# Optimization experiments

Measured on AMD Instinct MI355X. Metric: run time of the kernel, lower is better.

Reference implementation:

```python
import jax, jax.numpy as jnp
import numpy as np

N_NODES = 250_000
N_EDGES = 1_250_000
N_CRY = 50_000
EMB = 200
FEA = 64
HID = 256
N_GRAPH = 3
ELEM_HEADS = 3
CRY_HEADS = 3


def _simple_net(x, w1, b1, w2, b2):
    # SimpleNetwork([d_in, 256, d_out]): Linear -> LeakyReLU -> Linear
    h = jax.nn.leaky_relu(x @ w1 + b1, negative_slope=0.01)
    return h @ w2 + b2


def setup_inputs() -> dict:
    key = jax.random.key(0)
    ks = jax.random.split(key, 32)
    s = 0.05
    inp = {
        # weights strictly positive (fractional stoichiometry weights)
        "elem_weights": jax.random.uniform(ks[0], (N_NODES, 1), jnp.float32) * 0.9 + 0.05,
        "elem_fea": jax.random.normal(ks[1], (N_NODES, EMB), jnp.float32),
        "self_fea_idx": jax.random.randint(ks[2], (N_EDGES,), 0, N_NODES),
        "nbr_fea_idx": jax.random.randint(ks[3], (N_EDGES,), 0, N_NODES),
        "cry_elem_idx": jnp.sort(jax.random.randint(ks[4], (N_NODES,), 0, N_CRY)),
        # embedding: Linear(EMB, FEA-1)
        "emb_w": jax.random.normal(ks[5], (EMB, FEA - 1), jnp.float32) * s,
        "emb_b": jnp.zeros((FEA - 1,), jnp.float32),
        # graph-layer attention heads (n_graph, elem_heads, ...)
        "g_gate_w1": jax.random.normal(ks[6], (N_GRAPH, ELEM_HEADS, 2 * FEA, HID), jnp.float32) * s,
        "g_gate_b1": jnp.zeros((N_GRAPH, ELEM_HEADS, HID), jnp.float32),
        "g_gate_w2": jax.random.normal(ks[7], (N_GRAPH, ELEM_HEADS, HID, 1), jnp.float32) * s,
        "g_gate_b2": jnp.zeros((N_GRAPH, ELEM_HEADS, 1), jnp.float32),
        "g_msg_w1": jax.random.normal(ks[8], (N_GRAPH, ELEM_HEADS, 2 * FEA, HID), jnp.float32) * s,
        "g_msg_b1": jnp.zeros((N_GRAPH, ELEM_HEADS, HID), jnp.float32),
        "g_msg_w2": jax.random.normal(ks[9], (N_GRAPH, ELEM_HEADS, HID, FEA), jnp.float32) * s,
        "g_msg_b2": jnp.zeros((N_GRAPH, ELEM_HEADS, FEA), jnp.float32),
        "g_pow": jax.random.normal(ks[10], (N_GRAPH, ELEM_HEADS), jnp.float32),
        # crystal pooling heads
        "c_gate_w1": jax.random.normal(ks[11], (CRY_HEADS, FEA, HID), jnp.float32) * s,
        "c_gate_b1": jnp.zeros((CRY_HEADS, HID), jnp.float32),
        "c_gate_w2": jax.random.normal(ks[12], (CRY_HEADS, HID, 1), jnp.float32) * s,
        "c_gate_b2": jnp.zeros((CRY_HEADS, 1), jnp.float32),
        "c_msg_w1": jax.random.normal(ks[13], (CRY_HEADS, FEA, HID), jnp.float32) * s,
        "c_msg_b1": jnp.zeros((CRY_HEADS, HID), jnp.float32),
        "c_msg_w2": jax.random.normal(ks[14], (CRY_HEADS, HID, FEA), jnp.float32) * s,
        "c_msg_b2": jnp.zeros((CRY_HEADS, FEA), jnp.float32),
        "c_pow": jax.random.normal(ks[15], (CRY_HEADS,), jnp.float32),
    }
    return inp


def _attn_pool(fea, weights, index, num_segments, gw1, gb1, gw2, gb2, mw1, mb1, mw2, mb2, p):
    # WeightedAttentionPooling: scatter-softmax with (weights ** pow) factor
    gate = _simple_net(fea, gw1, gb1, gw2, gb2)                       # (E, 1)
    gmax = jax.ops.segment_max(gate, index, num_segments=num_segments)
    gate = (weights ** p) * jnp.exp(gate - gmax[index])
    den = jax.ops.segment_sum(gate, index, num_segments=num_segments)
    gate = gate / (den[index] + 1e-10)
    msg = _simple_net(fea, mw1, mb1, mw2, mb2)                        # (E, FEA)
    return jax.ops.segment_sum(gate * msg, index, num_segments=num_segments)


def reference(elem_weights, elem_fea, self_fea_idx, nbr_fea_idx, cry_elem_idx,
              emb_w, emb_b,
              g_gate_w1, g_gate_b1, g_gate_w2, g_gate_b2,
              g_msg_w1, g_msg_b1, g_msg_w2, g_msg_b2, g_pow,
              c_gate_w1, c_gate_b1, c_gate_w2, c_gate_b2,
              c_msg_w1, c_msg_b1, c_msg_w2, c_msg_b2, c_pow):
    n = elem_fea.shape[0]
    x = elem_fea @ emb_w + emb_b                                      # (N, FEA-1)
    x = jnp.concatenate([x, elem_weights], axis=1)                    # (N, FEA)
    w_nbr = elem_weights[nbr_fea_idx]                                 # (M, 1)
    for l in range(g_pow.shape[0]):
        fea = jnp.concatenate([x[self_fea_idx], x[nbr_fea_idx]], axis=1)  # (M, 2*FEA)
        heads = []
        for h in range(g_pow.shape[1]):
            heads.append(_attn_pool(
                fea, w_nbr, self_fea_idx, n,
                g_gate_w1[l, h], g_gate_b1[l, h], g_gate_w2[l, h], g_gate_b2[l, h],
                g_msg_w1[l, h], g_msg_b1[l, h], g_msg_w2[l, h], g_msg_b2[l, h],
                g_pow[l, h]))
        x = jnp.mean(jnp.stack(heads), axis=0) + x                    # residual
    heads = []
    for h in range(c_pow.shape[0]):
        heads.append(_attn_pool(
            x, elem_weights, cry_elem_idx, N_CRY,
            c_gate_w1[h], c_gate_b1[h], c_gate_w2[h], c_gate_b2[h],
            c_msg_w1[h], c_msg_b1[h], c_msg_w2[h], c_msg_b2[h],
            c_pow[h]))
    return jnp.mean(jnp.stack(heads), axis=0)                         # (C, FEA)
```

## Files before the change

kernel.cpp:

```cpp
#include <hip/hip_runtime.h>
#include <math.h>

#define NN 250000
#define NE 1250000
#define NC 50000
#define EMBD 200
#define NCH 245
#define NBLK 22000
#define SSTR ((size_t)NBLK * 64)

typedef unsigned int u32;
typedef unsigned short u16;
typedef short s16x8 __attribute__((ext_vector_type(8)));
typedef float f32x4 __attribute__((ext_vector_type(4)));

__device__ __forceinline__ u16 f2bf(float f) {
    u32 u = __float_as_uint(f);
    return (u16)((u + 0x7FFFu + ((u >> 16) & 1u)) >> 16);
}
__device__ __forceinline__ float bf2f(u16 u) { return __uint_as_float(((u32)u) << 16); }
__device__ __forceinline__ u32 cvtpk(float lo, float hi) {
    u32 r;
    asm("v_cvt_pk_bf16_f32 %0, %1, %2" : "=v"(r) : "v"(lo), "v"(hi));
    return r;
}
__device__ __forceinline__ float lrelu(float v) { return v > 0.f ? v : 0.01f * v; }
__device__ __forceinline__ u32 encf(float f) {
    u32 u = __float_as_uint(f);
    return (u & 0x80000000u) ? ~u : (u | 0x80000000u);
}
__device__ __forceinline__ float decf(u32 k) {
    return __uint_as_float((k & 0x80000000u) ? (k ^ 0x80000000u) : ~k);
}

__global__ void k_pack(const float* __restrict__ src, u16* __restrict__ dst,
                       int K, int N, int nheads)
{
    const int t = blockIdx.x * 256 + threadIdx.x;
    const int F = (K / 32) * (N / 16);
    if (t >= nheads * F * 64) return;
    const int lane = t & 63;
    const int fh = t >> 6;
    const int f = fh % F, head = fh / F;
    const int ng = f % (N / 16), ks = f / (N / 16);
    const int q = lane >> 4, c = lane & 15;
    const float* s = src + (size_t)head * K * N;
    u16 o[8];
    #pragma unroll
    for (int i = 0; i < 8; ++i)
        o[i] = f2bf(s[(size_t)(32 * ks + 8 * q + i) * N + 16 * ng + c]);
    uint4 v;
    v.x = (u32)o[0] | ((u32)o[1] << 16);
    v.y = (u32)o[2] | ((u32)o[3] << 16);
    v.z = (u32)o[4] | ((u32)o[5] << 16);
    v.w = (u32)o[6] | ((u32)o[7] << 16);
    *(uint4*)(dst + (size_t)head * K * N + ((size_t)f * 64 + lane) * 8) = v;
}

__global__ void k_packe(const float* __restrict__ src, u16* __restrict__ dst)
{
    const int t = blockIdx.x * 256 + threadIdx.x;
    if (t >= 28 * 64) return;
    const int lane = t & 63, f = t >> 6;
    const int ng = f & 3, ks = f >> 2;
    const int q = lane >> 4, c = lane & 15;
    u16 o[8];
    #pragma unroll
    for (int i = 0; i < 8; ++i) {
        const int kr = 32 * ks + 8 * q + i;
        const int col = 16 * ng + c;
        o[i] = (kr < EMBD && col < 63) ? f2bf(src[kr * 63 + col]) : (u16)0;
    }
    uint4 v;
    v.x = (u32)o[0] | ((u32)o[1] << 16);
    v.y = (u32)o[2] | ((u32)o[3] << 16);
    v.z = (u32)o[4] | ((u32)o[5] << 16);
    v.w = (u32)o[6] | ((u32)o[7] << 16);
    *(uint4*)(dst + ((size_t)f * 64 + lane) * 8) = v;
}

__global__ void k_pack2(const float* __restrict__ src, u16* __restrict__ dst, int nheads)
{
    const int t = blockIdx.x * 256 + threadIdx.x;
    const int F = 32;
    if (t >= nheads * F * 64) return;
    const int lane = t & 63;
    const int fh = t >> 6;
    const int f = fh % F, head = fh / F;
    const int ks2 = f >> 2, ng = f & 3;
    const int q = lane >> 4, c = lane & 15;
    const int half = ks2 >> 2, k2l = ks2 & 3;
    const float* s = src + (size_t)head * 256 * 64;
    u16 o[8];
    #pragma unroll
    for (int i = 0; i < 8; ++i) {
        const int pl = 32 * k2l + 8 * q + i;
        const int krow = (pl >> 5) * 64 + (2 * half + (pl & 1)) * 16 + ((pl >> 1) & 15);
        o[i] = f2bf(s[(size_t)krow * 64 + 16 * ng + c]);
    }
    uint4 v;
    v.x = (u32)o[0] | ((u32)o[1] << 16);
    v.y = (u32)o[2] | ((u32)o[3] << 16);
    v.z = (u32)o[4] | ((u32)o[5] << 16);
    v.w = (u32)o[6] | ((u32)o[7] << 16);
    *(uint4*)(dst + (size_t)head * 256 * 64 + ((size_t)f * 64 + lane) * 8) = v;
}

__global__ __launch_bounds__(256) void k_embed_mm(
    const float* __restrict__ elem_fea, const float* __restrict__ elem_w,
    const u16* __restrict__ webp, const float* __restrict__ emb_b,
    float* __restrict__ x, u16* __restrict__ xbf)
{
    __shared__ __align__(16) u16 Ahi[64 * 256];
    __shared__ __align__(16) u16 Alo[64 * 256];
    const int tid = threadIdx.x;
    const int n0 = blockIdx.x * 64;

    for (int i = tid; i < 64 * 3; i += 256) {
        const int row = i / 3, j = 25 + i % 3;
        uint4 z; z.x = 0; z.y = 0; z.z = 0; z.w = 0;
        *(uint4*)((char*)Ahi + row * 512 + ((j ^ (row & 7)) * 16)) = z;
        *(uint4*)((char*)Alo + row * 512 + ((j ^ (row & 7)) * 16)) = z;
    }
    for (int i = tid; i < 64 * 50; i += 256) {
        const int row = i / 50, f4 = i % 50;
        const int node = min(n0 + row, NN - 1);
        float4 v = *(const float4*)(elem_fea + (size_t)node * EMBD + f4 * 4);
        const u16 h0 = f2bf(v.x), h1 = f2bf(v.y), h2 = f2bf(v.z), h3 = f2bf(v.w);
        uint2 hi, lo;
        hi.x = (u32)h0 | ((u32)h1 << 16);
        hi.y = (u32)h2 | ((u32)h3 << 16);
        lo.x = (u32)f2bf(v.x - bf2f(h0)) | ((u32)f2bf(v.y - bf2f(h1)) << 16);
        lo.y = (u32)f2bf(v.z - bf2f(h2)) | ((u32)f2bf(v.w - bf2f(h3)) << 16);
        const int off = row * 512 + (((f4 >> 1) ^ (row & 7)) * 16) + (f4 & 1) * 8;
        *(uint2*)((char*)Ahi + off) = hi;
        *(uint2*)((char*)Alo + off) = lo;
    }
    __syncthreads();

    const int w = tid >> 6, lane = tid & 63, q = lane >> 4, c = lane & 15;
    s16x8 B[7];
    #pragma unroll
    for (int ks = 0; ks < 7; ++ks)
        B[ks] = *(const s16x8*)(webp + ((size_t)(ks * 4 + w) * 64 + lane) * 8);
    f32x4 acc[4];
    #pragma unroll
    for (int m = 0; m < 4; ++m) acc[m] = 0.f;
    #pragma unroll
    for (int ks = 0; ks < 7; ++ks) {
        #pragma unroll
        for (int m = 0; m < 4; ++m) {
            const int row = m * 16 + c;
            const int g = (ks * 4 + q) ^ (row & 7);
            s16x8 ah = *(const s16x8*)((const char*)Ahi + row * 512 + g * 16);
            s16x8 al = *(const s16x8*)((const char*)Alo + row * 512 + g * 16);
            acc[m] = __builtin_amdgcn_mfma_f32_16x16x32_bf16(ah, B[ks], acc[m], 0, 0, 0);
            acc[m] = __builtin_amdgcn_mfma_f32_16x16x32_bf16(al, B[ks], acc[m], 0, 0, 0);
        }
    }
    const int col = w * 16 + c;
    const float bv = (col < 63) ? emb_b[col] : 0.f;
    #pragma unroll
    for (int m = 0; m < 4; ++m)
        #pragma unroll
        for (int r = 0; r < 4; ++r) {
            const int node = n0 + m * 16 + q * 4 + r;
            if (node < NN) {
                const float val = (col < 63) ? acc[m][r] + bv : elem_w[node];
                x[(size_t)node * 64 + col] = val;
                xbf[(size_t)node * 64 + col] = f2bf(val);
            }
        }
}

__global__ void k_deg(const int* __restrict__ self_idx, int* __restrict__ deg) {
    int e = blockIdx.x * 256 + threadIdx.x;
    if (e < NE) atomicAdd(&deg[self_idx[e]], 1);
}

__global__ void k_nodepack(const int* __restrict__ deg, int* __restrict__ nstart,
                           int* __restrict__ ctotal)
{
    __shared__ int sdeg[1024];
    __shared__ int sst[1024];
    const int c0 = blockIdx.x << 10;
    const int cnt = min(1024, NN - c0);
    for (int i = threadIdx.x; i < cnt; i += 64) sdeg[i] = deg[c0 + i];
    __syncthreads();
    if (threadIdx.x == 0) {
        int cur = 0;
        for (int i = 0; i < cnt; ++i) {
            int d = sdeg[i];
            if (d > 0 && ((cur & 63) + d > 64)) cur = (cur + 63) & ~63;
            sst[i] = cur;
            cur += d;
        }
        ctotal[blockIdx.x] = (cur + 63) & ~63;
    }
    __syncthreads();
    for (int i = threadIdx.x; i < cnt; i += 64) nstart[c0 + i] = sst[i];
}

__global__ void k_chunkscan(const int* __restrict__ ctotal, int* __restrict__ cbase) {
    __shared__ int s[256];
    int t = threadIdx.x;
    int v = (t < NCH) ? ctotal[t] : 0;
    s[t] = v;
    __syncthreads();
    for (int off = 1; off < 256; off <<= 1) {
        int add = (t >= off) ? s[t - off] : 0;
        __syncthreads();
        s[t] += add;
        __syncthreads();
    }
    if (t < NCH) cbase[t] = s[t] - v;
}

__global__ void k_fill(const int* __restrict__ self_idx, const int* __restrict__ nstart,
                       const int* __restrict__ cbase, int* __restrict__ cursor,
                       int* __restrict__ eslot)
{
    int e = blockIdx.x * 256 + threadIdx.x;
    if (e >= NE) return;
    int n = self_idx[e];
    int r = atomicAdd(&cursor[n], 1);
    eslot[cbase[n >> 10] + nstart[n] + r] = e;
}

__global__ __launch_bounds__(256, 4) void k_lgate(
    const u16* __restrict__ xbf, const int* __restrict__ eslot,
    const int* __restrict__ sidx, const int* __restrict__ nidx,
    const float* __restrict__ elem_w,
    const u16* __restrict__ gw1p, const float* __restrict__ gb1,
    const float* __restrict__ gw2, const float* __restrict__ gpw,
    float* __restrict__ sgf_out)
{
    __shared__ __align__(16) u16 sA[64 * 128];
    __shared__ float sg[4][64];
    __shared__ float gfin[64], tval[64];
    __shared__ float swn[64];
    __shared__ int   snid[64];
    __shared__ short srs[64], sre[64];
    const int tid = threadIdx.x;
    const int base = blockIdx.x * 64;
    if (eslot[base] < 0) return;

    if (tid < 64) {
        int e = eslot[base + tid];
        snid[tid] = (e >= 0) ? sidx[e] : -1;
        swn[tid] = (e >= 0) ? elem_w[nidx[e]] : 1.f;
    }
    for (int i = tid; i < 64 * 16; i += 256) {
        const int row = i >> 4, g = i & 15;
        const int e = eslot[base + row];
        uint4 v; v.x = 0; v.y = 0; v.z = 0; v.w = 0;
        if (e >= 0) {
            const int node = (g < 8) ? sidx[e] : nidx[e];
            v = *(const uint4*)(xbf + (size_t)node * 64 + (g & 7) * 8);
        }
        *(uint4*)((char*)sA + row * 256 + ((g ^ (row & 7)) * 16)) = v;
    }
    __syncthreads();
    if (tid < 64) {
        int n = snid[tid];
        int rs = tid, re = tid + 1;
        if (n >= 0) {
            while (rs > 0 && snid[rs - 1] == n) --rs;
            while (re < 64 && snid[re] == n) ++re;
        }
        srs[tid] = (short)rs; sre[tid] = (short)re;
    }

    const int w = tid >> 6, lane = tid & 63, q = lane >> 4, c = lane & 15;

    #pragma unroll 1
    for (int h = 0; h < 3; ++h) {
        float part[4][4];
        #pragma unroll
        for (int m = 0; m < 4; ++m)
            #pragma unroll
            for (int r = 0; r < 4; ++r) part[m][r] = 0.f;
        const u16* wp = gw1p + (size_t)h * 128 * 256;
        #pragma unroll 1
        for (int half = 0; half < 2; ++half) {
            f32x4 acc[4][2];
            #pragma unroll
            for (int m = 0; m < 4; ++m) { acc[m][0] = 0.f; acc[m][1] = 0.f; }
            __builtin_amdgcn_s_setprio(1);
            #pragma unroll 2
            for (int ks = 0; ks < 4; ++ks) {
                s16x8 B1[2];
                #pragma unroll
                for (int n2 = 0; n2 < 2; ++n2)
                    B1[n2] = *(const s16x8*)(wp + ((size_t)(ks * 16 + w * 4 + half * 2 + n2) * 64 + lane) * 8);
                s16x8 a[4];
                #pragma unroll
                for (int m = 0; m < 4; ++m) {
                    const int row = m * 16 + c;
                    a[m] = *(const s16x8*)((const char*)sA + row * 256 + (((ks * 4 + q) ^ (row & 7)) * 16));
                }
                #pragma unroll
                for (int n2 = 0; n2 < 2; ++n2)
                    #pragma unroll
                    for (int m = 0; m < 4; ++m)
                        acc[m][n2] = __builtin_amdgcn_mfma_f32_16x16x32_bf16(a[m], B1[n2], acc[m][n2], 0, 0, 0);
            }
            __builtin_amdgcn_s_setprio(0);
            #pragma unroll
            for (int n2 = 0; n2 < 2; ++n2) {
                const int col = w * 64 + (half * 2 + n2) * 16 + c;
                const float b1v = gb1[h * 256 + col];
                const float w2v = gw2[h * 256 + col];
                #pragma unroll
                for (int m = 0; m < 4; ++m)
                    #pragma unroll
                    for (int r = 0; r < 4; ++r)
                        part[m][r] += lrelu(acc[m][n2][r] + b1v) * w2v;
            }
        }
        #pragma unroll
        for (int off = 1; off < 16; off <<= 1)
            #pragma unroll
            for (int m = 0; m < 4; ++m)
                #pragma unroll
                for (int r = 0; r < 4; ++r)
                    part[m][r] += __shfl_xor(part[m][r], off, 64);
        if (c == 0) {
            #pragma unroll
            for (int m = 0; m < 4; ++m)
                #pragma unroll
                for (int r = 0; r < 4; ++r)
                    sg[w][m * 16 + q * 4 + r] = part[m][r];
        }
        __syncthreads();
        if (tid < 64)
            gfin[tid] = (snid[tid] >= 0) ? sg[0][tid] + sg[1][tid] + sg[2][tid] + sg[3][tid] : -1e30f;
        __syncthreads();
        if (tid < 64) {
            const int rs = srs[tid], re = sre[tid];
            float m = -1e30f;
            for (int j = rs; j < re; ++j) m = fmaxf(m, gfin[j]);
            tval[tid] = (snid[tid] >= 0) ? powf(swn[tid], gpw[h]) * expf(gfin[tid] - m) : 0.f;
        }
        __syncthreads();
        if (tid < 64) {
            const int rs = srs[tid], re = sre[tid];
            float d = 1e-10f;
            for (int j = rs; j < re; ++j) d += tval[j];
            sgf_out[SSTR * h + base + tid] = tval[tid] / d;
        }
        __syncthreads();
    }
}

__global__ __launch_bounds__(256, 4) void k_lmsg(
    const u16* __restrict__ xbf, const int* __restrict__ eslot,
    const int* __restrict__ sidx, const int* __restrict__ nidx,
    const u16* __restrict__ mw1p, const float* __restrict__ mb1,
    const u16* __restrict__ mw2p, const float* __restrict__ mb2,
    const float* __restrict__ sgf_in, float* __restrict__ pooled)
{
    __shared__ __align__(16) u16 sA[64 * 128];
    __shared__ __align__(16) u16 sH[64 * 128];
    __shared__ float sgfl[64][3];
    __shared__ int   snid[64];
    __shared__ short srs[64], sre[64];
    const int tid = threadIdx.x;
    const int base = blockIdx.x * 64;
    if (eslot[base] < 0) return;

    if (tid < 64) {
        int e = eslot[base + tid];
        snid[tid] = (e >= 0) ? sidx[e] : -1;
    }
    if (tid < 192) {
        const int row = tid / 3, h = tid % 3;
        sgfl[row][h] = sgf_in[SSTR * h + base + row];
    }
    for (int i = tid; i < 64 * 16; i += 256) {
        const int row = i >> 4, g = i & 15;
        const int e = eslot[base + row];
        uint4 v; v.x = 0; v.y = 0; v.z = 0; v.w = 0;
        if (e >= 0) {
            const int node = (g < 8) ? sidx[e] : nidx[e];
            v = *(const uint4*)(xbf + (size_t)node * 64 + (g & 7) * 8);
        }
        *(uint4*)((char*)sA + row * 256 + ((g ^ (row & 7)) * 16)) = v;
    }
    __syncthreads();
    if (tid < 64) {
        int n = snid[tid];
        int rs = tid, re = tid + 1;
        if (n >= 0) {
            while (rs > 0 && snid[rs - 1] == n) --rs;
            while (re < 64 && snid[re] == n) ++re;
        }
        srs[tid] = (short)rs; sre[tid] = (short)re;
    }

    const int w = tid >> 6, lane = tid & 63, q = lane >> 4, c = lane & 15;
    float wacc[4][4];
    #pragma unroll
    for (int m = 0; m < 4; ++m)
        #pragma unroll
        for (int r = 0; r < 4; ++r) wacc[m][r] = 0.f;

    #pragma unroll 1
    for (int h = 0; h < 3; ++h) {
        const u16* wp = mw1p + (size_t)h * 128 * 256;
        #pragma unroll 1
        for (int half = 0; half < 2; ++half) {
            f32x4 acc[4][2];
            #pragma unroll
            for (int m = 0; m < 4; ++m) { acc[m][0] = 0.f; acc[m][1] = 0.f; }
            __builtin_amdgcn_s_setprio(1);
            #pragma unroll 2
            for (int ks = 0; ks < 4; ++ks) {
                s16x8 B1[2];
                #pragma unroll
                for (int n2 = 0; n2 < 2; ++n2)
                    B1[n2] = *(const s16x8*)(wp + ((size_t)(ks * 16 + w * 4 + half * 2 + n2) * 64 + lane) * 8);
                s16x8 a[4];
                #pragma unroll
                for (int m = 0; m < 4; ++m) {
                    const int row = m * 16 + c;
                    a[m] = *(const s16x8*)((const char*)sA + row * 256 + (((ks * 4 + q) ^ (row & 7)) * 16));
                }
                #pragma unroll
                for (int n2 = 0; n2 < 2; ++n2)
                    #pragma unroll
                    for (int m = 0; m < 4; ++m)
                        acc[m][n2] = __builtin_amdgcn_mfma_f32_16x16x32_bf16(a[m], B1[n2], acc[m][n2], 0, 0, 0);
            }
            __builtin_amdgcn_s_setprio(0);

            __syncthreads();
            const float b1a = mb1[h * 256 + w * 64 + (half * 2 + 0) * 16 + c];
            const float b1b = mb1[h * 256 + w * 64 + (half * 2 + 1) * 16 + c];
            #pragma unroll
            for (int m = 0; m < 4; ++m)
                #pragma unroll
                for (int r = 0; r < 4; ++r) {
                    const int row = m * 16 + q * 4 + r;
                    const u32 pk = cvtpk(lrelu(acc[m][0][r] + b1a), lrelu(acc[m][1][r] + b1b));
                    *(u32*)((char*)sH + row * 256 + (((w * 4 + (c >> 2)) ^ (row & 7)) * 16) + (c & 3) * 4) = pk;
                }
            s16x8 B2[4];
            #pragma unroll
            for (int k2 = 0; k2 < 4; ++k2)
                B2[k2] = *(const s16x8*)(mw2p + (size_t)h * 256 * 64 + ((size_t)((half * 4 + k2) * 4 + w) * 64 + lane) * 8);
            __syncthreads();

            f32x4 acc2[4];
            #pragma unroll
            for (int m = 0; m < 4; ++m) acc2[m] = 0.f;
            __builtin_amdgcn_s_setprio(1);
            #pragma unroll
            for (int k2 = 0; k2 < 4; ++k2) {
                #pragma unroll
                for (int m2 = 0; m2 < 4; ++m2) {
                    const int row = m2 * 16 + c;
                    s16x8 a2 = *(const s16x8*)((const char*)sH + row * 256 + (((k2 * 4 + q) ^ (row & 7)) * 16));
                    acc2[m2] = __builtin_amdgcn_mfma_f32_16x16x32_bf16(a2, B2[k2], acc2[m2], 0, 0, 0);
                }
            }
            __builtin_amdgcn_s_setprio(0);
            const float b2v = half ? mb2[h * 64 + w * 16 + c] : 0.f;
            #pragma unroll
            for (int m2 = 0; m2 < 4; ++m2)
                #pragma unroll
                for (int r = 0; r < 4; ++r) {
                    const int row = m2 * 16 + q * 4 + r;
                    wacc[m2][r] += (acc2[m2][r] + b2v) * sgfl[row][h];
                }
        }
        __syncthreads();
    }

    float* waccL = (float*)sH;
    #pragma unroll
    for (int m = 0; m < 4; ++m)
        #pragma unroll
        for (int r = 0; r < 4; ++r)
            waccL[(m * 16 + q * 4 + r) * 64 + w * 16 + c] = wacc[m][r];
    __syncthreads();
    {
        const int col = tid & 63, grp = tid >> 6;
        for (int i = grp; i < 64; i += 4) {
            const int n = snid[i];
            if (n >= 0 && srs[i] == (short)i) {
                float s = 0.f;
                const int re = sre[i];
                for (int j = i; j < re; ++j) s += waccL[j * 64 + col];
                pooled[(size_t)n * 64 + col] = s * (1.f / 3.f);
            }
        }
    }
}

__global__ void k_mirror2(float* __restrict__ x, const float* __restrict__ pooled,
                          u16* __restrict__ xbf, int n4)
{
    int i = blockIdx.x * 256 + threadIdx.x;
    if (i >= n4) return;
    float4 xv = *(const float4*)(x + (size_t)i * 4);
    float4 pv = *(const float4*)(pooled + (size_t)i * 4);
    xv.x += pv.x; xv.y += pv.y; xv.z += pv.z; xv.w += pv.w;
    *(float4*)(x + (size_t)i * 4) = xv;
    uint2 o;
    o.x = cvtpk(xv.x, xv.y);
    o.y = cvtpk(xv.z, xv.w);
    *(uint2*)(xbf + (size_t)i * 4) = o;
}

template<int KD, bool GATHER>
__global__ __launch_bounds__(256, 4) void k_gate(
    const u16* __restrict__ xbf, const int* __restrict__ sidx, const int* __restrict__ nidx,
    const int* __restrict__ scat, const u16* __restrict__ w1p,
    const float* __restrict__ b1g, const float* __restrict__ w2g,
    float* __restrict__ gate_out, u32* __restrict__ gmax, int nrows, size_t gstride)
{
    constexpr int KS = KD / 32;
    constexpr int RB = KD * 2;
    constexpr int G  = KD / 8;
    __shared__ __align__(16) u16 sA[64 * KD];
    __shared__ float sg[4][64];
    const int tid = threadIdx.x;
    const int r0 = blockIdx.x * 64;
    const int rem = min(64, nrows - r0);

    for (int i = tid; i < 64 * G; i += 256) {
        const int row = i / G, g = i % G;
        const int rr = (row < rem) ? row : 0;
        uint4 v;
        if (GATHER) {
            const int node = (g < G / 2) ? sidx[r0 + rr] : nidx[r0 + rr];
            v = *(const uint4*)(xbf + (size_t)node * 64 + (g & (G / 2 - 1)) * 8);
        } else {
            v = *(const uint4*)(xbf + (size_t)(r0 + rr) * 64 + g * 8);
        }
        *(uint4*)((char*)sA + row * RB + ((g ^ (row & 7)) * 16)) = v;
    }
    __syncthreads();

    const int w = tid >> 6, lane = tid & 63, q = lane >> 4, c = lane & 15;

    #pragma unroll 1
    for (int h = 0; h < 3; ++h) {
        float part[4][4];
        #pragma unroll
        for (int m = 0; m < 4; ++m)
            #pragma unroll
            for (int r = 0; r < 4; ++r) part[m][r] = 0.f;
        const u16* wp = w1p + (size_t)h * KD * 256;
        #pragma unroll 1
        for (int half = 0; half < 2; ++half) {
            f32x4 acc[4][2];
            #pragma unroll
            for (int m = 0; m < 4; ++m) { acc[m][0] = 0.f; acc[m][1] = 0.f; }
            __builtin_amdgcn_s_setprio(1);
            #pragma unroll 2
            for (int ks = 0; ks < KS; ++ks) {
                s16x8 B1[2];
                #pragma unroll
                for (int n2 = 0; n2 < 2; ++n2)
                    B1[n2] = *(const s16x8*)(wp + ((size_t)(ks * 16 + w * 4 + half * 2 + n2) * 64 + lane) * 8);
                s16x8 a[4];
                #pragma unroll
                for (int m = 0; m < 4; ++m) {
                    const int row = m * 16 + c;
                    a[m] = *(const s16x8*)((const char*)sA + row * RB + (((ks * 4 + q) ^ (row & 7)) * 16));
                }
                #pragma unroll
                for (int n2 = 0; n2 < 2; ++n2)
                    #pragma unroll
                    for (int m = 0; m < 4; ++m)
                        acc[m][n2] = __builtin_amdgcn_mfma_f32_16x16x32_bf16(a[m], B1[n2], acc[m][n2], 0, 0, 0);
            }
            __builtin_amdgcn_s_setprio(0);
            #pragma unroll
            for (int n2 = 0; n2 < 2; ++n2) {
                const int col = w * 64 + (half * 2 + n2) * 16 + c;
                const float b1v = b1g[h * 256 + col];
                const float w2v = w2g[h * 256 + col];
                #pragma unroll
                for (int m = 0; m < 4; ++m)
                    #pragma unroll
                    for (int r = 0; r < 4; ++r)
                        part[m][r] += lrelu(acc[m][n2][r] + b1v) * w2v;
            }
        }
        #pragma unroll
        for (int off = 1; off < 16; off <<= 1)
            #pragma unroll
            for (int m = 0; m < 4; ++m)
                #pragma unroll
                for (int r = 0; r < 4; ++r)
                    part[m][r] += __shfl_xor(part[m][r], off, 64);
        if (c == 0) {
            #pragma unroll
            for (int m = 0; m < 4; ++m)
                #pragma unroll
                for (int r = 0; r < 4; ++r)
                    sg[w][m * 16 + q * 4 + r] = part[m][r];
        }
        __syncthreads();
        if (tid < rem) {
            const float gv = sg[0][tid] + sg[1][tid] + sg[2][tid] + sg[3][tid];
            gate_out[gstride * h + r0 + tid] = gv;
            atomicMax(&gmax[scat[r0 + tid] * 3 + h], encf(gv));
        }
        __syncthreads();
    }
}

template<int KD, bool GATHER>
__global__ __launch_bounds__(256, 4) void k_msg(
    const u16* __restrict__ xbf, const int* __restrict__ sidx, const int* __restrict__ nidx,
    const int* __restrict__ scat, const u16* __restrict__ w1p, const float* __restrict__ b1g,
    const u16* __restrict__ w2p, const float* __restrict__ b2g,
    const float* __restrict__ tbuf, const float* __restrict__ den,
    float* __restrict__ outp, int nrows, size_t gstride)
{
    constexpr int KS = KD / 32;
    constexpr int RB = KD * 2;
    constexpr int G  = KD / 8;
    __shared__ __align__(16) u16 sA[64 * KD];
    __shared__ __align__(16) u16 sH[64 * 128];
    __shared__ float sgf[64][3];
    __shared__ int ssi[64];
    const int tid = threadIdx.x;
    const int r0 = blockIdx.x * 64;
    const int rem = min(64, nrows - r0);

    for (int i = tid; i < 64 * G; i += 256) {
        const int row = i / G, g = i % G;
        const int rr = (row < rem) ? row : 0;
        uint4 v;
        if (GATHER) {
            const int node = (g < G / 2) ? sidx[r0 + rr] : nidx[r0 + rr];
            v = *(const uint4*)(xbf + (size_t)node * 64 + (g & (G / 2 - 1)) * 8);
        } else {
            v = *(const uint4*)(xbf + (size_t)(r0 + rr) * 64 + g * 8);
        }
        *(uint4*)((char*)sA + row * RB + ((g ^ (row & 7)) * 16)) = v;
    }
    if (tid < 64) ssi[tid] = (tid < rem) ? scat[r0 + tid] : 0;
    if (tid < 192) {
        const int row = tid / 3, h = tid % 3;
        if (row < rem) {
            const int s = scat[r0 + row] * 3 + h;
            sgf[row][h] = tbuf[gstride * h + r0 + row] / (den[s] + 1e-10f);
        } else {
            sgf[row][h] = 0.f;
        }
    }
    __syncthreads();

    const int w = tid >> 6, lane = tid & 63, q = lane >> 4, c = lane & 15;
    float wacc[4][4];
    #pragma unroll
    for (int m = 0; m < 4; ++m)
        #pragma unroll
        for (int r = 0; r < 4; ++r) wacc[m][r] = 0.f;

    #pragma unroll 1
    for (int h = 0; h < 3; ++h) {
        const u16* wp = w1p + (size_t)h * KD * 256;
        #pragma unroll 1
        for (int half = 0; half < 2; ++half) {
            f32x4 acc[4][2];
            #pragma unroll
            for (int m = 0; m < 4; ++m) { acc[m][0] = 0.f; acc[m][1] = 0.f; }
            __builtin_amdgcn_s_setprio(1);
            #pragma unroll 2
            for (int ks = 0; ks < KS; ++ks) {
                s16x8 B1[2];
                #pragma unroll
                for (int n2 = 0; n2 < 2; ++n2)
                    B1[n2] = *(const s16x8*)(wp + ((size_t)(ks * 16 + w * 4 + half * 2 + n2) * 64 + lane) * 8);
                s16x8 a[4];
                #pragma unroll
                for (int m = 0; m < 4; ++m) {
                    const int row = m * 16 + c;
                    a[m] = *(const s16x8*)((const char*)sA + row * RB + (((ks * 4 + q) ^ (row & 7)) * 16));
                }
                #pragma unroll
                for (int n2 = 0; n2 < 2; ++n2)
                    #pragma unroll
                    for (int m = 0; m < 4; ++m)
                        acc[m][n2] = __builtin_amdgcn_mfma_f32_16x16x32_bf16(a[m], B1[n2], acc[m][n2], 0, 0, 0);
            }
            __builtin_amdgcn_s_setprio(0);

            __syncthreads();
            const float b1a = b1g[h * 256 + w * 64 + (half * 2 + 0) * 16 + c];
            const float b1b = b1g[h * 256 + w * 64 + (half * 2 + 1) * 16 + c];
            #pragma unroll
            for (int m = 0; m < 4; ++m)
                #pragma unroll
                for (int r = 0; r < 4; ++r) {
                    const int row = m * 16 + q * 4 + r;
                    const u32 pk = cvtpk(lrelu(acc[m][0][r] + b1a), lrelu(acc[m][1][r] + b1b));
                    *(u32*)((char*)sH + row * 256 + (((w * 4 + (c >> 2)) ^ (row & 7)) * 16) + (c & 3) * 4) = pk;
                }
            s16x8 B2[4];
            #pragma unroll
            for (int k2 = 0; k2 < 4; ++k2)
                B2[k2] = *(const s16x8*)(w2p + (size_t)h * 256 * 64 + ((size_t)((half * 4 + k2) * 4 + w) * 64 + lane) * 8);
            __syncthreads();

            f32x4 acc2[4];
            #pragma unroll
            for (int m = 0; m < 4; ++m) acc2[m] = 0.f;
            __builtin_amdgcn_s_setprio(1);
            #pragma unroll
            for (int k2 = 0; k2 < 4; ++k2) {
                #pragma unroll
                for (int m2 = 0; m2 < 4; ++m2) {
                    const int row = m2 * 16 + c;
                    s16x8 a2 = *(const s16x8*)((const char*)sH + row * 256 + (((k2 * 4 + q) ^ (row & 7)) * 16));
                    acc2[m2] = __builtin_amdgcn_mfma_f32_16x16x32_bf16(a2, B2[k2], acc2[m2], 0, 0, 0);
                }
            }
            __builtin_amdgcn_s_setprio(0);
            const float b2v = half ? b2g[h * 64 + w * 16 + c] : 0.f;
            #pragma unroll
            for (int m2 = 0; m2 < 4; ++m2)
                #pragma unroll
                for (int r = 0; r < 4; ++r) {
                    const int row = m2 * 16 + q * 4 + r;
                    wacc[m2][r] += (acc2[m2][r] + b2v) * sgf[row][h];
                }
        }
    }
    #pragma unroll
    for (int m = 0; m < 4; ++m)
        #pragma unroll
        for (int r = 0; r < 4; ++r) {
            const int row = m * 16 + q * 4 + r;
            if (row < rem)
                atomicAdd(&outp[(size_t)ssi[row] * 64 + w * 16 + c], wacc[m][r] * (1.f / 3.f));
        }
}

__global__ void k_seg_exp(float* __restrict__ gate_t, const int* __restrict__ idx,
                          const int* __restrict__ wi, const float* __restrict__ elem_w,
                          const float* __restrict__ pw, const u32* __restrict__ gmax,
                          float* __restrict__ den, int n, size_t gstride)
{
    int e = blockIdx.x * blockDim.x + threadIdx.x;
    if (e >= n) return;
    int s = idx[e] * 3;
    float wgt = elem_w[wi ? wi[e] : e];
    #pragma unroll
    for (int h = 0; h < 3; ++h) {
        float gm = decf(gmax[s + h]);
        float t = powf(wgt, pw[h]) * expf(gate_t[gstride * h + e] - gm);
        gate_t[gstride * h + e] = t;
        atomicAdd(&den[s + h], t);
    }
}

extern "C" void kernel_launch(void* const* d_in, const int* in_sizes, int n_in,
                              void* d_out, int out_size, void* d_ws, size_t ws_size,
                              hipStream_t stream)
{
    const float* elem_w   = (const float*)d_in[0];
    const float* elem_fea = (const float*)d_in[1];
    const int*   self_idx = (const int*)d_in[2];
    const int*   nbr_idx  = (const int*)d_in[3];
    const int*   cry_idx  = (const int*)d_in[4];
    const float* emb_w    = (const float*)d_in[5];
    const float* emb_b    = (const float*)d_in[6];
    const float* gg_w1    = (const float*)d_in[7];
    const float* gg_b1    = (const float*)d_in[8];
    const float* gg_w2    = (const float*)d_in[9];
    const float* gm_w1    = (const float*)d_in[11];
    const float* gm_b1    = (const float*)d_in[12];
    const float* gm_w2    = (const float*)d_in[13];
    const float* gm_b2    = (const float*)d_in[14];
    const float* g_pow    = (const float*)d_in[15];
    const float* cg_w1    = (const float*)d_in[16];
    const float* cg_b1    = (const float*)d_in[17];
    const float* cg_w2    = (const float*)d_in[18];
    const float* cm_w1    = (const float*)d_in[20];
    const float* cm_b1    = (const float*)d_in[21];
    const float* cm_w2    = (const float*)d_in[22];
    const float* cm_b2    = (const float*)d_in[23];
    const float* c_pow    = (const float*)d_in[24];

    char* wsp = (char*)d_ws;
    size_t off = 0;
    auto alloc = [&](size_t b) { char* p = wsp + off; off += (b + 255) & ~(size_t)255; return p; };
    float* x      = (float*)alloc((size_t)NN * 64 * 4);
    float* pooled = (float*)alloc((size_t)NN * 64 * 4);
    u16*   xbf    = (u16*)  alloc((size_t)NN * 64 * 2);
    float* sgf    = (float*)alloc((size_t)3 * SSTR * 4);
    float* gate_t = (float*)alloc((size_t)NN * 3 * 4);
    float* cden   = (float*)alloc((size_t)NC * 3 * 4);
    u32*   cgmax  = (u32*)  alloc((size_t)NC * 3 * 4);
    int* deg    = (int*)alloc((size_t)NN * 4);
    int* nstart = (int*)alloc((size_t)NN * 4);
    int* cursor = (int*)alloc((size_t)NN * 4);
    int* ctotal = (int*)alloc((size_t)NCH * 4);
    int* cbase  = (int*)alloc((size_t)NCH * 4);
    int* eslot  = (int*)alloc((size_t)NBLK * 64 * 4);
    u16* wg1p = (u16*)alloc((size_t)9 * 128 * 256 * 2);
    u16* wm1p = (u16*)alloc((size_t)9 * 128 * 256 * 2);
    u16* wm2p = (u16*)alloc((size_t)9 * 256 * 64 * 2);
    u16* cg1p = (u16*)alloc((size_t)3 * 64 * 256 * 2);
    u16* cm1p = (u16*)alloc((size_t)3 * 64 * 256 * 2);
    u16* cm2p = (u16*)alloc((size_t)3 * 256 * 64 * 2);
    u16* webp = (u16*)alloc((size_t)224 * 64 * 2);

    auto pack = [&](const float* s, u16* d, int K, int N, int H) {
        int tot = H * (K / 32) * (N / 16) * 64;
        k_pack<<<(tot + 255) / 256, 256, 0, stream>>>(s, d, K, N, H);
    };
    pack(gg_w1, wg1p, 128, 256, 9);
    pack(gm_w1, wm1p, 128, 256, 9);
    pack(cg_w1, cg1p, 64, 256, 3);
    pack(cm_w1, cm1p, 64, 256, 3);
    k_pack2<<<(9 * 32 * 64 + 255) / 256, 256, 0, stream>>>(gm_w2, wm2p, 9);
    k_pack2<<<(3 * 32 * 64 + 255) / 256, 256, 0, stream>>>(cm_w2, cm2p, 3);
    k_packe<<<7, 256, 0, stream>>>(emb_w, webp);

    hipMemsetAsync(deg, 0, (size_t)NN * 4, stream);
    hipMemsetAsync(cursor, 0, (size_t)NN * 4, stream);
    hipMemsetAsync(eslot, 0xFF, (size_t)NBLK * 64 * 4, stream);
    k_deg<<<(NE + 255) / 256, 256, 0, stream>>>(self_idx, deg);
    k_nodepack<<<NCH, 64, 0, stream>>>(deg, nstart, ctotal);
    k_chunkscan<<<1, 256, 0, stream>>>(ctotal, cbase);
    k_fill<<<(NE + 255) / 256, 256, 0, stream>>>(self_idx, nstart, cbase, cursor, eslot);

    k_embed_mm<<<(NN + 63) / 64, 256, 0, stream>>>(elem_fea, elem_w, webp, emb_b, x, xbf);

    for (int l = 0; l < 3; ++l) {
        hipMemsetAsync(pooled, 0, (size_t)NN * 64 * 4, stream);
        k_lgate<<<NBLK, 256, 0, stream>>>(
            xbf, eslot, self_idx, nbr_idx, elem_w,
            wg1p + (size_t)l * 3 * 128 * 256, gg_b1 + l * 768, gg_w2 + l * 768, g_pow + l * 3,
            sgf);
        k_lmsg<<<NBLK, 256, 0, stream>>>(
            xbf, eslot, self_idx, nbr_idx,
            wm1p + (size_t)l * 3 * 128 * 256, gm_b1 + l * 768,
            wm2p + (size_t)l * 3 * 256 * 64, gm_b2 + l * 192, sgf, pooled);
        k_mirror2<<<(NN * 64 / 4 + 255) / 256, 256, 0, stream>>>(x, pooled, xbf, NN * 64 / 4);
    }

    hipMemsetAsync(cgmax, 0, (size_t)NC * 3 * 4, stream);
    hipMemsetAsync(cden, 0, (size_t)NC * 3 * 4, stream);
    hipMemsetAsync(d_out, 0, (size_t)NC * 64 * 4, stream);
    const int GN = (NN + 63) / 64;
    k_gate<64, false><<<GN, 256, 0, stream>>>(
        xbf, nullptr, nullptr, cry_idx, cg1p, cg_b1, cg_w2, gate_t, cgmax, NN, (size_t)NN);
    k_seg_exp<<<(NN + 255) / 256, 256, 0, stream>>>(
        gate_t, cry_idx, nullptr, elem_w, c_pow, cgmax, cden, NN, (size_t)NN);
    k_msg<64, false><<<GN, 256, 0, stream>>>(
        xbf, nullptr, nullptr, cry_idx, cm1p, cm_b1, cm2p, cm_b2,
        gate_t, cden, (float*)d_out, NN, (size_t)NN);
}
```

Before: 4.237 ms.

## Compute gate second layer with MFMA and precompute edge node indices

The gate kernel's second linear layer (256 to 1) is now done with MFMA instructions. Hidden activations are staged to shared memory as bf16, and the 256-to-1 weights are packed into an MFMA B-operand layout (replicated across columns). This replaces the scalar lrelu-multiply accumulation and the cross-lane shuffle reduction. Separately, the fill kernel writes sorted (self, neighbour) node pairs and neighbour weights directly, removing the double indirection through edge ids in both layer kernels. The change adds two block barriers per half-iteration and bf16 rounding of the hidden layer before the gate dot product.

```diff
diff --git a/kernel.cpp b/kernel.cpp
--- a/kernel.cpp
+++ b/kernel.cpp
@@ -104,6 +104,30 @@
     v.z = (u32)o[4] | ((u32)o[5] << 16);
     v.w = (u32)o[6] | ((u32)o[7] << 16);
     *(uint4*)(dst + (size_t)head * 256 * 64 + ((size_t)f * 64 + lane) * 8) = v;
+}
+
+__global__ void k_packg(const float* __restrict__ src, u16* __restrict__ dst, int nheads)
+{
+    const int t = blockIdx.x * 256 + threadIdx.x;
+    if (t >= nheads * 8 * 64) return;
+    const int lane = t & 63;
+    const int fh = t >> 6;
+    const int f = fh & 7, head = fh >> 3;
+    const int half = f >> 2, k2l = f & 3;
+    const int q = lane >> 4;
+    u16 o[8];
+    #pragma unroll
+    for (int i = 0; i < 8; ++i) {
+        const int pl = 32 * k2l + 8 * q + i;
+        const int krow = (pl >> 5) * 64 + (2 * half + (pl & 1)) * 16 + ((pl >> 1) & 15);
+        o[i] = f2bf(src[head * 256 + krow]);
+    }
+    uint4 v;
+    v.x = (u32)o[0] | ((u32)o[1] << 16);
+    v.y = (u32)o[2] | ((u32)o[3] << 16);
+    v.z = (u32)o[4] | ((u32)o[5] << 16);
+    v.w = (u32)o[6] | ((u32)o[7] << 16);
+    *(uint4*)(dst + ((size_t)(head * 8 + f) * 64 + lane) * 8) = v;
 }
 
 __global__ __launch_bounds__(256) void k_embed_mm(
@@ -216,26 +240,31 @@
     if (t < NCH) cbase[t] = s[t] - v;
 }
 
-__global__ void k_fill(const int* __restrict__ self_idx, const int* __restrict__ nstart,
-                       const int* __restrict__ cbase, int* __restrict__ cursor,
-                       int* __restrict__ eslot)
+__global__ void k_fill(const int* __restrict__ self_idx, const int* __restrict__ nbr_idx,
+                       const float* __restrict__ elem_w,
+                       const int* __restrict__ nstart, const int* __restrict__ cbase,
+                       int* __restrict__ cursor, int2* __restrict__ gnode,
+                       float* __restrict__ gwn)
 {
     int e = blockIdx.x * 256 + threadIdx.x;
     if (e >= NE) return;
     int n = self_idx[e];
     int r = atomicAdd(&cursor[n], 1);
-    eslot[cbase[n >> 10] + nstart[n] + r] = e;
+    int slot = cbase[n >> 10] + nstart[n] + r;
+    int nb = nbr_idx[e];
+    gnode[slot] = make_int2(n, nb);
+    gwn[slot] = elem_w[nb];
 }
 
 __global__ __launch_bounds__(256, 4) void k_lgate(
-    const u16* __restrict__ xbf, const int* __restrict__ eslot,
-    const int* __restrict__ sidx, const int* __restrict__ nidx,
-    const float* __restrict__ elem_w,
+    const u16* __restrict__ xbf, const int2* __restrict__ gnode,
+    const float* __restrict__ gwn,
     const u16* __restrict__ gw1p, const float* __restrict__ gb1,
-    const float* __restrict__ gw2, const float* __restrict__ gpw,
+    const u16* __restrict__ gw2p, const float* __restrict__ gpw,
     float* __restrict__ sgf_out)
 {
     __shared__ __align__(16) u16 sA[64 * 128];
+    __shared__ __align__(16) u16 sH[64 * 128];
     __shared__ float sg[4][64];
     __shared__ float gfin[64], tval[64];
     __shared__ float swn[64];
@@ -243,21 +272,19 @@
     __shared__ short srs[64], sre[64];
     const int tid = threadIdx.x;
     const int base = blockIdx.x * 64;
-    if (eslot[base] < 0) return;
+    if (gnode[base].x < 0) return;
 
     if (tid < 64) {
-        int e = eslot[base + tid];
-        snid[tid] = (e >= 0) ? sidx[e] : -1;
-        swn[tid] = (e >= 0) ? elem_w[nidx[e]] : 1.f;
+        int2 nn = gnode[base + tid];
+        snid[tid] = nn.x;
+        swn[tid] = gwn[base + tid];
     }
     for (int i = tid; i < 64 * 16; i += 256) {
         const int row = i >> 4, g = i & 15;
-        const int e = eslot[base + row];
+        const int2 nn = gnode[base + row];
+        const int node = (g < 8) ? nn.x : nn.y;
         uint4 v; v.x = 0; v.y = 0; v.z = 0; v.w = 0;
-        if (e >= 0) {
-            const int node = (g < 8) ? sidx[e] : nidx[e];
-            v = *(const uint4*)(xbf + (size_t)node * 64 + (g & 7) * 8);
-        }
+        if (node >= 0) v = *(const uint4*)(xbf + (size_t)node * 64 + (g & 7) * 8);
         *(uint4*)((char*)sA + row * 256 + ((g ^ (row & 7)) * 16)) = v;
     }
     __syncthreads();
@@ -275,11 +302,9 @@
 
     #pragma unroll 1
     for (int h = 0; h < 3; ++h) {
-        float part[4][4];
+        f32x4 acc2[4];
         #pragma unroll
-        for (int m = 0; m < 4; ++m)
-            #pragma unroll
-            for (int r = 0; r < 4; ++r) part[m][r] = 0.f;
+        for (int m = 0; m < 4; ++m) acc2[m] = 0.f;
         const u16* wp = gw1p + (size_t)h * 128 * 256;
         #pragma unroll 1
         for (int half = 0; half < 2; ++half) {
@@ -306,31 +331,36 @@
                         acc[m][n2] = __builtin_amdgcn_mfma_f32_16x16x32_bf16(a[m], B1[n2], acc[m][n2], 0, 0, 0);
             }
             __builtin_amdgcn_s_setprio(0);
-            #pragma unroll
-            for (int n2 = 0; n2 < 2; ++n2) {
-                const int col = w * 64 + (half * 2 + n2) * 16 + c;
-                const float b1v = gb1[h * 256 + col];
-                const float w2v = gw2[h * 256 + col];
-                #pragma unroll
-                for (int m = 0; m < 4; ++m)
-                    #pragma unroll
-                    for (int r = 0; r < 4; ++r)
-                        part[m][r] += lrelu(acc[m][n2][r] + b1v) * w2v;
-            }
-        }
-        #pragma unroll
-        for (int off = 1; off < 16; off <<= 1)
+
+            __syncthreads();
+            const float b1a = gb1[h * 256 + w * 64 + (half * 2 + 0) * 16 + c];
+            const float b1b = gb1[h * 256 + w * 64 + (half * 2 + 1) * 16 + c];
             #pragma unroll
             for (int m = 0; m < 4; ++m)
                 #pragma unroll
+                for (int r = 0; r < 4; ++r) {
+                    const int row = m * 16 + q * 4 + r;
+                    const u32 pk = cvtpk(lrelu(acc[m][0][r] + b1a), lrelu(acc[m][1][r] + b1b));
+                    *(u32*)((char*)sH + row * 256 + (((w * 4 + (c >> 2)) ^ (row & 7)) * 16) + (c & 3) * 4) = pk;
+                }
+            s16x8 B2 = *(const s16x8*)(gw2p + ((size_t)(h * 8 + half * 4 + w) * 64 + lane) * 8);
+            __syncthreads();
+
+            __builtin_amdgcn_s_setprio(1);
+            #pragma unroll
+            for (int m = 0; m < 4; ++m) {
+                const int row = m * 16 + c;
+                s16x8 a2 = *(const s16x8*)((const char*)sH + row * 256 + (((w * 4 + q) ^ (row & 7)) * 16));
+                acc2[m] = __builtin_amdgcn_mfma_f32_16x16x32_bf16(a2, B2, acc2[m], 0, 0, 0);
+            }
+            __builtin_amdgcn_s_setprio(0);
+        }
+        if (c == 0) {
+            #pragma unroll
+            for (int m = 0; m < 4; ++m)
+                #pragma unroll
                 for (int r = 0; r < 4; ++r)
-                    part[m][r] += __shfl_xor(part[m][r], off, 64);
-        if (c == 0) {
-            #pragma unroll
-            for (int m = 0; m < 4; ++m)
-                #pragma unroll
-                for (int r = 0; r < 4; ++r)
-                    sg[w][m * 16 + q * 4 + r] = part[m][r];
+                    sg[w][m * 16 + q * 4 + r] = acc2[m][r];
         }
         __syncthreads();
         if (tid < 64)
@@ -354,8 +384,7 @@
 }
 
 __global__ __launch_bounds__(256, 4) void k_lmsg(
-    const u16* __restrict__ xbf, const int* __restrict__ eslot,
-    const int* __restrict__ sidx, const int* __restrict__ nidx,
+    const u16* __restrict__ xbf, const int2* __restrict__ gnode,
     const u16* __restrict__ mw1p, const float* __restrict__ mb1,
     const u16* __restrict__ mw2p, const float* __restrict__ mb2,
     const float* __restrict__ sgf_in, float* __restrict__ pooled)
@@ -367,24 +396,19 @@
     __shared__ short srs[64], sre[64];
     const int tid = threadIdx.x;
     const int base = blockIdx.x * 64;
-    if (eslot[base] < 0) return;
-
-    if (tid < 64) {
-        int e = eslot[base + tid];
-        snid[tid] = (e >= 0) ? sidx[e] : -1;
-    }
+    if (gnode[base].x < 0) return;
+
+    if (tid < 64) snid[tid] = gnode[base + tid].x;
     if (tid < 192) {
         const int row = tid / 3, h = tid % 3;
         sgfl[row][h] = sgf_in[SSTR * h + base + row];
     }
     for (int i = tid; i < 64 * 16; i += 256) {
         const int row = i >> 4, g = i & 15;
-        const int e = eslot[base + row];
+        const int2 nn = gnode[base + row];
+        const int node = (g < 8) ? nn.x : nn.y;
         uint4 v; v.x = 0; v.y = 0; v.z = 0; v.w = 0;
-        if (e >= 0) {
-            const int node = (g < 8) ? sidx[e] : nidx[e];
-            v = *(const uint4*)(xbf + (size_t)node * 64 + (g & 7) * 8);
-        }
+        if (node >= 0) v = *(const uint4*)(xbf + (size_t)node * 64 + (g & 7) * 8);
         *(uint4*)((char*)sA + row * 256 + ((g ^ (row & 7)) * 16)) = v;
     }
     __syncthreads();
@@ -805,10 +829,12 @@
     int* cursor = (int*)alloc((size_t)NN * 4);
     int* ctotal = (int*)alloc((size_t)NCH * 4);
     int* cbase  = (int*)alloc((size_t)NCH * 4);
-    int* eslot  = (int*)alloc((size_t)NBLK * 64 * 4);
+    int2* gnode = (int2*)alloc((size_t)NBLK * 64 * 8);
+    float* gwn  = (float*)alloc((size_t)NBLK * 64 * 4);
     u16* wg1p = (u16*)alloc((size_t)9 * 128 * 256 * 2);
     u16* wm1p = (u16*)alloc((size_t)9 * 128 * 256 * 2);
     u16* wm2p = (u16*)alloc((size_t)9 * 256 * 64 * 2);
+    u16* wg2p = (u16*)alloc((size_t)9 * 8 * 64 * 8 * 2);
     u16* cg1p = (u16*)alloc((size_t)3 * 64 * 256 * 2);
     u16* cm1p = (u16*)alloc((size_t)3 * 64 * 256 * 2);
     u16* cm2p = (u16*)alloc((size_t)3 * 256 * 64 * 2);
@@ -824,26 +850,28 @@
     pack(cm_w1, cm1p, 64, 256, 3);
     k_pack2<<<(9 * 32 * 64 + 255) / 256, 256, 0, stream>>>(gm_w2, wm2p, 9);
     k_pack2<<<(3 * 32 * 64 + 255) / 256, 256, 0, stream>>>(cm_w2, cm2p, 3);
+    k_packg<<<(9 * 8 * 64 + 255) / 256, 256, 0, stream>>>(gg_w2, wg2p, 9);
     k_packe<<<7, 256, 0, stream>>>(emb_w, webp);
 
     hipMemsetAsync(deg, 0, (size_t)NN * 4, stream);
     hipMemsetAsync(cursor, 0, (size_t)NN * 4, stream);
-    hipMemsetAsync(eslot, 0xFF, (size_t)NBLK * 64 * 4, stream);
+    hipMemsetAsync(gnode, 0xFF, (size_t)NBLK * 64 * 8, stream);
     k_deg<<<(NE + 255) / 256, 256, 0, stream>>>(self_idx, deg);
     k_nodepack<<<NCH, 64, 0, stream>>>(deg, nstart, ctotal);
     k_chunkscan<<<1, 256, 0, stream>>>(ctotal, cbase);
-    k_fill<<<(NE + 255) / 256, 256, 0, stream>>>(self_idx, nstart, cbase, cursor, eslot);
+    k_fill<<<(NE + 255) / 256, 256, 0, stream>>>(self_idx, nbr_idx, elem_w,
+                                                 nstart, cbase, cursor, gnode, gwn);
 
     k_embed_mm<<<(NN + 63) / 64, 256, 0, stream>>>(elem_fea, elem_w, webp, emb_b, x, xbf);
 
     for (int l = 0; l < 3; ++l) {
         hipMemsetAsync(pooled, 0, (size_t)NN * 64 * 4, stream);
         k_lgate<<<NBLK, 256, 0, stream>>>(
-            xbf, eslot, self_idx, nbr_idx, elem_w,
-            wg1p + (size_t)l * 3 * 128 * 256, gg_b1 + l * 768, gg_w2 + l * 768, g_pow + l * 3,
-            sgf);
+            xbf, gnode, gwn,
+            wg1p + (size_t)l * 3 * 128 * 256, gg_b1 + l * 768,
+            wg2p + (size_t)l * 3 * 8 * 64 * 8, g_pow + l * 3, sgf);
         k_lmsg<<<NBLK, 256, 0, stream>>>(
-            xbf, eslot, self_idx, nbr_idx,
+            xbf, gnode,
             wm1p + (size_t)l * 3 * 128 * 256, gm_b1 + l * 768,
             wm2p + (size_t)l * 3 * 256 * 64, gm_b2 + l * 192, sgf, pooled);
         k_mirror2<<<(NN * 64 / 4 + 255) / 256, 256, 0, stream>>>(x, pooled, xbf, NN * 64 / 4);
```

Result: faster. 3.988 ms (median of 2 runs) (-5.9%).
